# Kernel optimization log

Hardware: AMD Instinct MI355X
Metric: run time of the kernel (lower is better)

The kernel has to match this reference:

```python
import jax, jax.numpy as jnp
import numpy as np

N_NODES = 100000
N_EDGES = 1000000
NEG_SLOPE = 0.2


def gat_conv(x, src, dst, W, al, ar, b, res, activation):
    """DGL-style GATConv. res is None (no residual), 'id' (identity residual), or a [in,H*D] matrix."""
    H, D = al.shape
    n = x.shape[0]
    feat = (x @ W).reshape(n, H, D)                      # [N,H,D]
    el = jnp.einsum('nhd,hd->nh', feat, al)              # [N,H]
    er = jnp.einsum('nhd,hd->nh', feat, ar)              # [N,H]
    e = jax.nn.leaky_relu(el[src] + er[dst], NEG_SLOPE)  # [E,H]
    # edge softmax over incoming edges of each dst node
    m = jax.lax.stop_gradient(jax.ops.segment_max(e, dst, num_segments=n))
    ex = jnp.exp(e - m[dst])
    s = jax.ops.segment_sum(ex, dst, num_segments=n)
    alpha = ex / s[dst]                                  # [E,H]
    out = jax.ops.segment_sum(feat[src] * alpha[:, :, None], dst, num_segments=n)  # [N,H,D]
    if res == 'id':
        out = out + x.reshape(n, H, D)
    elif res is not None:
        out = out + (x @ res).reshape(n, H, D)
    out = out + b.reshape(1, H, D)
    if activation is not None:
        out = activation(out)
    return out


def setup_inputs() -> dict:
    key = jax.random.key(0)
    ks = jax.random.split(key, 20)
    F_IN, HID = 128, 32
    H1, H2, H3 = 4, 4, 1
    C = 40
    sc = 0.1
    inp = {
        'x':   jax.random.normal(ks[0], (N_NODES, F_IN), dtype=jnp.float32),
        'src': jax.random.randint(ks[1], (N_EDGES,), 0, N_NODES, dtype=jnp.int32),
        'dst': jax.random.randint(ks[2], (N_EDGES,), 0, N_NODES, dtype=jnp.int32),
        # layer 1: in=128 -> H1*HID=128, no residual, elu
        'W1':  sc * jax.random.normal(ks[3], (F_IN, H1 * HID), dtype=jnp.float32),
        'al1': sc * jax.random.normal(ks[4], (H1, HID), dtype=jnp.float32),
        'ar1': sc * jax.random.normal(ks[5], (H1, HID), dtype=jnp.float32),
        'b1':  jnp.zeros((H1 * HID,), dtype=jnp.float32),
        # layer 2: in=128 -> H2*HID=128, identity residual, elu
        'W2':  sc * jax.random.normal(ks[6], (H1 * HID, H2 * HID), dtype=jnp.float32),
        'al2': sc * jax.random.normal(ks[7], (H2, HID), dtype=jnp.float32),
        'ar2': sc * jax.random.normal(ks[8], (H2, HID), dtype=jnp.float32),
        'b2':  jnp.zeros((H2 * HID,), dtype=jnp.float32),
        # layer 3 (output): in=128 -> H3*HID=32, projected residual, no activation
        'W3':  sc * jax.random.normal(ks[9], (H2 * HID, H3 * HID), dtype=jnp.float32),
        'al3': sc * jax.random.normal(ks[10], (H3, HID), dtype=jnp.float32),
        'ar3': sc * jax.random.normal(ks[11], (H3, HID), dtype=jnp.float32),
        'b3':  jnp.zeros((H3 * HID,), dtype=jnp.float32),
        'res3': sc * jax.random.normal(ks[12], (H2 * HID, H3 * HID), dtype=jnp.float32),
        # final classifier
        'Wfc': sc * jax.random.normal(ks[13], (HID, C), dtype=jnp.float32),
        'bfc': jnp.zeros((C,), dtype=jnp.float32),
    }
    return inp


def reference(x, src, dst, W1, al1, ar1, b1, W2, al2, ar2, b2, W3, al3, ar3, b3, res3, Wfc, bfc):
    n = x.shape[0]
    h = gat_conv(x, src, dst, W1, al1, ar1, b1, None, jax.nn.elu).reshape(n, -1)   # [N, 128]
    h = gat_conv(h, src, dst, W2, al2, ar2, b2, 'id', jax.nn.elu).reshape(n, -1)   # [N, 128]
    h = gat_conv(h, src, dst, W3, al3, ar3, b3, res3, None).mean(axis=1)           # [N, 32]
    return h @ Wfc + bfc                                                           # [N, 40]
```

## Files before the change

kernel.cpp:

```cpp
#include <hip/hip_runtime.h>
#include <cstdint>
#include <cstddef>

#define NN 100000
#define NE 1000000
#define GEMM_BLOCKS 1563
#define TICKET_BLOCKS 3907
#define CAST_BLOCKS 12500
#define LOG2E 1.4426950408896340736f

typedef unsigned int uint;
typedef unsigned short ushort;
typedef __attribute__((ext_vector_type(8))) short bfrag;
typedef __attribute__((ext_vector_type(4))) float f32x4;

__device__ __forceinline__ ushort f2bf(float f){
  uint u = __float_as_uint(f);
  u += 0x7fffu + ((u >> 16) & 1u);
  return (ushort)(u >> 16);
}
__device__ __forceinline__ float bflo(uint p){ return __uint_as_float(p << 16); }
__device__ __forceinline__ float bfhi(uint p){ return __uint_as_float(p & 0xffff0000u); }


__global__ __launch_bounds__(256) void k_scan_local(const int* __restrict__ cnt, int* __restrict__ rowptr,
                                                    int* __restrict__ bsum){
  __shared__ int sm[256];
  int t = threadIdx.x;
  int i = blockIdx.x*256 + t;
  int v = (i < NN) ? cnt[i] : 0;
  sm[t] = v;
  __syncthreads();
  for (int off=1; off<256; off<<=1){
    int u = (t>=off) ? sm[t-off] : 0;
    __syncthreads();
    sm[t] += u;
    __syncthreads();
  }
  if (i < NN) rowptr[i] = sm[t] - v;
  if (t == 255) bsum[blockIdx.x] = sm[255];
}

__global__ __launch_bounds__(512) void k_scan_bsum(const int* __restrict__ bsum, int* __restrict__ boff, int nb){
  __shared__ int sm[512];
  int t = threadIdx.x;
  int v = (t < nb) ? bsum[t] : 0;
  sm[t] = v;
  __syncthreads();
  for (int off=1; off<512; off<<=1){
    int u = (t>=off) ? sm[t-off] : 0;
    __syncthreads();
    sm[t] += u;
    __syncthreads();
  }
  if (t < nb) boff[t] = sm[t] - v;
}

__global__ __launch_bounds__(256) void k_scan_add(int* __restrict__ rowptr, const int* __restrict__ boff){
  int i = blockIdx.x*256 + threadIdx.x;
  if (i < NN) rowptr[i] += boff[i>>8];
  else if (i == NN) rowptr[NN] = NE;
}


__global__ __launch_bounds__(256) void k_dhist(const int* __restrict__ rowptr, int* __restrict__ dbin){
  __shared__ int lh[256];
  int t = threadIdx.x;
  lh[t] = 0;
  __syncthreads();
  int n = blockIdx.x*256 + t;
  if (n < NN){
    int deg = rowptr[n+1] - rowptr[n];
    atomicAdd(&lh[deg > 255 ? 255 : deg], 1);
  }
  __syncthreads();
  if (lh[t] > 0) atomicAdd(&dbin[t], lh[t]);
}

__global__ __launch_bounds__(256) void k_dscan(int* __restrict__ dbin){
  __shared__ int sm[256];
  int t = threadIdx.x;
  int v = dbin[t];
  sm[t] = v;
  __syncthreads();
  for (int off=1; off<256; off<<=1){
    int u = (t>=off) ? sm[t-off] : 0;
    __syncthreads();
    sm[t] += u;
    __syncthreads();
  }
  dbin[t] = sm[t] - v;
}

__global__ __launch_bounds__(256) void k_dscat(const int* __restrict__ rowptr, int* __restrict__ dbin,
                                               int* __restrict__ perm){
  __shared__ int lh[256];
  __shared__ int lbase[256];
  int t = threadIdx.x;
  lh[t] = 0;
  __syncthreads();
  int n = blockIdx.x*256 + t;
  int bin = -1, lticket = 0;
  if (n < NN){
    int deg = rowptr[n+1] - rowptr[n];
    bin = deg > 255 ? 255 : deg;
    lticket = atomicAdd(&lh[bin], 1);
  }
  __syncthreads();
  if (lh[t] > 0) lbase[t] = atomicAdd(&dbin[t], lh[t]);
  __syncthreads();
  if (n < NN) perm[lbase[bin] + lticket] = n;
}


__device__ __forceinline__ void bfrag_body(const float* __restrict__ B1, const float* __restrict__ B2,
                                           int n1, int n2, int NT, ushort* __restrict__ out, int i){
  if (i >= NT*4*64) return;
  int l = i & 63, ks = (i>>6)&3, nt = i>>8;
  int col = nt*16 + (l&15);
  int k0  = ks*32 + (l>>4)*8;
  const float* B; int stride, c;
  if (col < n1){ B = B1; stride = n1; c = col; }
  else         { B = B2; stride = n2; c = col - n1; }
  ushort v[8];
  #pragma unroll
  for (int j=0;j<8;j++) v[j] = f2bf(B[(size_t)(k0+j)*stride + c]);
  uint4 pk;
  pk.x = (uint)v[0] | ((uint)v[1]<<16);
  pk.y = (uint)v[2] | ((uint)v[3]<<16);
  pk.z = (uint)v[4] | ((uint)v[5]<<16);
  pk.w = (uint)v[6] | ((uint)v[7]<<16);
  *(uint4*)(out + (size_t)i*8) = pk;
}

__global__ __launch_bounds__(256) void k_prep(const float* __restrict__ x, ushort* __restrict__ xb,
                                              const float* __restrict__ W1, const float* __restrict__ W2,
                                              const float* __restrict__ W3, const float* __restrict__ res3,
                                              ushort* __restrict__ Bf1, ushort* __restrict__ Bf2,
                                              ushort* __restrict__ Bf3,
                                              const int* __restrict__ dst, int* __restrict__ cnt,
                                              int* __restrict__ tick){
  int bid = blockIdx.x, t = threadIdx.x;
  if (bid < CAST_BLOCKS){
    int i = bid*256 + t;
    float4 v = ((const float4*)x)[i];
    uint2 p;
    p.x = (uint)f2bf(v.x) | ((uint)f2bf(v.y)<<16);
    p.y = (uint)f2bf(v.z) | ((uint)f2bf(v.w)<<16);
    ((uint2*)xb)[i] = p;
  } else if (bid < CAST_BLOCKS + 20){
    int r = bid - CAST_BLOCKS;
    if (r < 8)       bfrag_body(W1, nullptr, 128, 0, 8, Bf1, r*256 + t);
    else if (r < 16) bfrag_body(W2, nullptr, 128, 0, 8, Bf2, (r-8)*256 + t);
    else             bfrag_body(W3, res3,    32, 32, 4, Bf3, (r-16)*256 + t);
  } else {
    int e = (bid - CAST_BLOCKS - 20)*256 + t;
    if (e < NE) tick[e] = atomicAdd(&cnt[dst[e]], 1);
  }
}


template<int NT, int NTF, int H>
__device__ __forceinline__ void gemm_body(int bid, const ushort* __restrict__ Ab, const ushort* __restrict__ Bf,
                                          ushort* __restrict__ featb, float* __restrict__ Cres,
                                          const float* __restrict__ al, const float* __restrict__ ar,
                                          float* __restrict__ el, float* __restrict__ er, int M){
  __shared__ ushort Bs[NT*2048];
  int t = threadIdx.x;
  #pragma unroll
  for (int i=0; i<NT; ++i)
    ((uint4*)Bs)[i*256 + t] = ((const uint4*)Bf)[i*256 + t];
  __syncthreads();

  int l = t & 63, w = t >> 6;
  int rw = bid*64 + w*16;
  int c = l & 15, g = l >> 4;

  f32x4 acc[NT];
  #pragma unroll
  for (int nt=0;nt<NT;nt++) acc[nt] = (f32x4){0.f,0.f,0.f,0.f};

  int rowA = rw + c; if (rowA >= M) rowA = M-1;
  const ushort* Ap = Ab + (size_t)rowA*128 + g*8;
  const bfrag* Bp = (const bfrag*)Bs;

  #pragma unroll
  for (int ks=0; ks<4; ++ks){
    bfrag a = *(const bfrag*)(Ap + ks*32);
    #pragma unroll
    for (int nt=0; nt<NT; ++nt){
      bfrag b = Bp[(nt*4+ks)*64 + l];
      acc[nt] = __builtin_amdgcn_mfma_f32_16x16x32_bf16(a, b, acc[nt], 0, 0, 0);
    }
  }

  float alv[H][2], arv[H][2];
  #pragma unroll
  for (int h=0;h<H;h++){
    alv[h][0]=al[h*32+c]*LOG2E;    arv[h][0]=ar[h*32+c]*LOG2E;
    alv[h][1]=al[h*32+16+c]*LOG2E; arv[h][1]=ar[h*32+16+c]*LOG2E;
  }

  #pragma unroll
  for (int reg=0; reg<4; ++reg){
    int row = rw + g*4 + reg;
    bool ok = row < M;
    #pragma unroll
    for (int h=0;h<H;h++){
      float pl = acc[2*h][reg]*alv[h][0] + acc[2*h+1][reg]*alv[h][1];
      float pr = acc[2*h][reg]*arv[h][0] + acc[2*h+1][reg]*arv[h][1];
      #pragma unroll
      for (int off=1; off<16; off<<=1){ pl += __shfl_xor(pl,off); pr += __shfl_xor(pr,off); }
      if (ok && c==0){ el[(size_t)row*H + h] = pl; er[(size_t)row*H + h] = pr; }
    }
    if (ok){
      #pragma unroll
      for (int nt=0; nt<NTF; ++nt)
        featb[(size_t)row*(NTF*16) + nt*16 + c] = f2bf(acc[nt][reg]);
      #pragma unroll
      for (int nt=NTF; nt<NT; ++nt)
        Cres[(size_t)row*((NT-NTF)*16) + (nt-NTF)*16 + c] = acc[nt][reg];
    }
  }
}

template<int NT, int NTF, int H>
__global__ __launch_bounds__(256) void k_gemm_mfma(const ushort* __restrict__ Ab, const ushort* __restrict__ Bf,
                                                   ushort* __restrict__ featb, float* __restrict__ Cres,
                                                   const float* __restrict__ al, const float* __restrict__ ar,
                                                   float* __restrict__ el, float* __restrict__ er, int M){
  gemm_body<NT,NTF,H>(blockIdx.x, Ab, Bf, featb, Cres, al, ar, el, er, M);
}

__global__ __launch_bounds__(256) void k_gemm1_place(const ushort* __restrict__ xb, const ushort* __restrict__ Bf1,
                                                     ushort* __restrict__ featb,
                                                     const float* __restrict__ al, const float* __restrict__ ar,
                                                     float* __restrict__ el, float* __restrict__ er,
                                                     const int* __restrict__ src, const int* __restrict__ dst,
                                                     const int* __restrict__ rowptr, const int* __restrict__ tick,
                                                     int* __restrict__ csr){
  int bid = blockIdx.x;
  if (bid < GEMM_BLOCKS){
    gemm_body<8,8,4>(bid, xb, Bf1, featb, nullptr, al, ar, el, er, NN);
  } else {
    int e = (bid - GEMM_BLOCKS)*256 + threadIdx.x;
    if (e < NE){
      int d = dst[e];
      csr[rowptr[d] + tick[e]] = src[e];
    }
  }
}


template<int RK>
__global__ __launch_bounds__(256) void k_agg4(const int* __restrict__ rowptr, const int* __restrict__ csr,
                                              const int* __restrict__ perm,
                                              const ushort* __restrict__ feat,
                                              const float* __restrict__ el, const float* __restrict__ er,
                                              const void* __restrict__ res, const float* __restrict__ bias,
                                              ushort* __restrict__ out, int act){
  int t = threadIdx.x;
  int l15 = t & 15;
  int node = perm[blockIdx.x*16 + (t>>4)];

  int beg = rowptr[node], deg = rowptr[node+1] - beg;
  int hm = l15 >> 2;
  float erh = er[(size_t)node*4 + hm];
  const int* cp = csr + beg;
  uint fo = (uint)l15*8u;

  float ssum = 0.f;
  float a0=0.f,a1=0.f,a2=0.f,a3=0.f,a4=0.f,a5=0.f,a6=0.f,a7=0.f;

  int ei = 0;
  for (; ei+2 <= deg; ei += 2){
    int s0 = cp[ei], s1 = cp[ei+1];
    uint4 p0 = *(const uint4*)(feat + ((uint)s0*128u + fo));
    uint4 p1 = *(const uint4*)(feat + ((uint)s1*128u + fo));
    float v0 = el[(uint)s0*4u + hm] + erh; v0 = fmaxf(v0, 0.2f*v0);
    float v1 = el[(uint)s1*4u + hm] + erh; v1 = fmaxf(v1, 0.2f*v1);
    float w0 = __builtin_amdgcn_exp2f(v0);
    float w1 = __builtin_amdgcn_exp2f(v1);
    ssum += w0 + w1;
    a0 += w0*bflo(p0.x) + w1*bflo(p1.x);
    a1 += w0*bfhi(p0.x) + w1*bfhi(p1.x);
    a2 += w0*bflo(p0.y) + w1*bflo(p1.y);
    a3 += w0*bfhi(p0.y) + w1*bfhi(p1.y);
    a4 += w0*bflo(p0.z) + w1*bflo(p1.z);
    a5 += w0*bfhi(p0.z) + w1*bfhi(p1.z);
    a6 += w0*bflo(p0.w) + w1*bflo(p1.w);
    a7 += w0*bfhi(p0.w) + w1*bfhi(p1.w);
  }
  if (ei < deg){
    int s0 = cp[ei];
    uint4 p0 = *(const uint4*)(feat + ((uint)s0*128u + fo));
    float v0 = el[(uint)s0*4u + hm] + erh; v0 = fmaxf(v0, 0.2f*v0);
    float w0 = __builtin_amdgcn_exp2f(v0);
    ssum += w0;
    a0 += w0*bflo(p0.x); a1 += w0*bfhi(p0.x);
    a2 += w0*bflo(p0.y); a3 += w0*bfhi(p0.y);
    a4 += w0*bflo(p0.z); a5 += w0*bfhi(p0.z);
    a6 += w0*bflo(p0.w); a7 += w0*bfhi(p0.w);
  }

  float inv = (deg > 0) ? 1.f/ssum : 0.f;
  float o0=a0*inv, o1=a1*inv, o2=a2*inv, o3=a3*inv;
  float o4=a4*inv, o5=a5*inv, o6=a6*inv, o7=a7*inv;
  if (RK == 1){
    uint4 rv = *(const uint4*)((const ushort*)res + (size_t)node*128 + fo);
    o0 += bflo(rv.x); o1 += bfhi(rv.x); o2 += bflo(rv.y); o3 += bfhi(rv.y);
    o4 += bflo(rv.z); o5 += bfhi(rv.z); o6 += bflo(rv.w); o7 += bfhi(rv.w);
  }
  float4 bv0 = *(const float4*)(bias + l15*8);
  float4 bv1 = *(const float4*)(bias + l15*8 + 4);
  o0 += bv0.x; o1 += bv0.y; o2 += bv0.z; o3 += bv0.w;
  o4 += bv1.x; o5 += bv1.y; o6 += bv1.z; o7 += bv1.w;
  if (act){
    o0 = (o0>0.f)?o0:__expf(o0)-1.f;
    o1 = (o1>0.f)?o1:__expf(o1)-1.f;
    o2 = (o2>0.f)?o2:__expf(o2)-1.f;
    o3 = (o3>0.f)?o3:__expf(o3)-1.f;
    o4 = (o4>0.f)?o4:__expf(o4)-1.f;
    o5 = (o5>0.f)?o5:__expf(o5)-1.f;
    o6 = (o6>0.f)?o6:__expf(o6)-1.f;
    o7 = (o7>0.f)?o7:__expf(o7)-1.f;
  }
  uint4 pk;
  pk.x = (uint)f2bf(o0) | ((uint)f2bf(o1)<<16);
  pk.y = (uint)f2bf(o2) | ((uint)f2bf(o3)<<16);
  pk.z = (uint)f2bf(o4) | ((uint)f2bf(o5)<<16);
  pk.w = (uint)f2bf(o6) | ((uint)f2bf(o7)<<16);
  *(uint4*)(out + (size_t)node*128 + fo) = pk;
}


__global__ __launch_bounds__(256) void k_agg1(const int* __restrict__ rowptr, const int* __restrict__ csr,
                                              const int* __restrict__ perm,
                                              const ushort* __restrict__ feat,
                                              const float* __restrict__ el, const float* __restrict__ er,
                                              const float* __restrict__ res, const float* __restrict__ bias,
                                              float* __restrict__ h3){
  int t = threadIdx.x;
  int l7 = t & 7;
  int node = perm[blockIdx.x*32 + (t>>3)];

  int beg = rowptr[node], deg = rowptr[node+1] - beg;
  float er0 = er[node];
  const int* cp = csr + beg;
  uint fo = (uint)l7*4u;

  float ssum = 0.f, a0=0.f, a1=0.f, a2=0.f, a3=0.f;
  int ei = 0;
  for (; ei+2 <= deg; ei += 2){
    int s0 = cp[ei], s1 = cp[ei+1];
    uint2 p0 = *(const uint2*)(feat + ((uint)s0*32u + fo));
    uint2 p1 = *(const uint2*)(feat + ((uint)s1*32u + fo));
    float v0 = el[s0] + er0; v0 = fmaxf(v0, 0.2f*v0);
    float v1 = el[s1] + er0; v1 = fmaxf(v1, 0.2f*v1);
    float w0 = __builtin_amdgcn_exp2f(v0);
    float w1 = __builtin_amdgcn_exp2f(v1);
    ssum += w0 + w1;
    a0 += w0*bflo(p0.x) + w1*bflo(p1.x);
    a1 += w0*bfhi(p0.x) + w1*bfhi(p1.x);
    a2 += w0*bflo(p0.y) + w1*bflo(p1.y);
    a3 += w0*bfhi(p0.y) + w1*bfhi(p1.y);
  }
  if (ei < deg){
    int s0 = cp[ei];
    uint2 p0 = *(const uint2*)(feat + ((uint)s0*32u + fo));
    float v0 = el[s0] + er0; v0 = fmaxf(v0, 0.2f*v0);
    float w0 = __builtin_amdgcn_exp2f(v0);
    ssum += w0;
    a0 += w0*bflo(p0.x); a1 += w0*bfhi(p0.x);
    a2 += w0*bflo(p0.y); a3 += w0*bfhi(p0.y);
  }

  float inv = (deg > 0) ? 1.f/ssum : 0.f;
  float4 rv = *(const float4*)(res + (size_t)node*32 + fo);
  float4 bv = *(const float4*)(bias + fo);
  float4 ov;
  ov.x = a0*inv + rv.x + bv.x;
  ov.y = a1*inv + rv.y + bv.y;
  ov.z = a2*inv + rv.z + bv.z;
  ov.w = a3*inv + rv.w + bv.w;
  *(float4*)(h3 + (size_t)node*32 + fo) = ov;
}


__global__ __launch_bounds__(256) void k_fc(const float* __restrict__ h, const float* __restrict__ W,
                                            const float* __restrict__ b, float* __restrict__ out){
  __shared__ float Ws[32*40];
  __shared__ float Hs[64][33];
  __shared__ float bs[40];
  int t = threadIdx.x;
  for (int i=t; i<1280; i+=256) Ws[i] = W[i];
  if (t < 40) bs[t] = b[t];
  int n0 = blockIdx.x*64;
  for (int idx=t; idx<512; idx+=256){
    int r = idx>>3, c4 = idx&7;
    float4 v;
    if (n0 + r < NN) v = *(const float4*)(h + (size_t)(n0+r)*32 + c4*4);
    else v = make_float4(0.f,0.f,0.f,0.f);
    Hs[r][c4*4+0]=v.x; Hs[r][c4*4+1]=v.y; Hs[r][c4*4+2]=v.z; Hs[r][c4*4+3]=v.w;
  }
  __syncthreads();
  int n = t>>2, cg = t&3;
  float acc[10];
  #pragma unroll
  for (int j=0;j<10;j++) acc[j] = 0.f;
  #pragma unroll
  for (int k=0;k<32;k++){
    float hv = Hs[n][k];
    #pragma unroll
    for (int j=0;j<10;j++) acc[j] += hv * Ws[k*40 + cg + 4*j];
  }
  int row = n0 + n;
  if (row < NN){
    #pragma unroll
    for (int j=0;j<10;j++) out[(size_t)row*40 + cg + 4*j] = acc[j] + bs[cg+4*j];
  }
}


extern "C" void kernel_launch(void* const* d_in, const int* in_sizes, int n_in,
                              void* d_out, int out_size, void* d_ws, size_t ws_size,
                              hipStream_t stream){
  const float* x    = (const float*)d_in[0];
  const int*   src  = (const int*)  d_in[1];
  const int*   dst  = (const int*)  d_in[2];
  const float* W1   = (const float*)d_in[3];
  const float* al1  = (const float*)d_in[4];
  const float* ar1  = (const float*)d_in[5];
  const float* b1   = (const float*)d_in[6];
  const float* W2   = (const float*)d_in[7];
  const float* al2  = (const float*)d_in[8];
  const float* ar2  = (const float*)d_in[9];
  const float* b2   = (const float*)d_in[10];
  const float* W3   = (const float*)d_in[11];
  const float* al3  = (const float*)d_in[12];
  const float* ar3  = (const float*)d_in[13];
  const float* b3   = (const float*)d_in[14];
  const float* res3 = (const float*)d_in[15];
  const float* Wfc  = (const float*)d_in[16];
  const float* bfc  = (const float*)d_in[17];
  float* out = (float*)d_out;

  char* ws = (char*)d_ws;
  size_t o = 0;
  auto alloc = [&](size_t bytes)->char*{
    char* p = ws + o;
    o += (bytes + 255) & ~(size_t)255;
    return p;
  };
  int*    rowptr = (int*)   alloc((size_t)(NN+1)*4);
  int*    cnt    = (int*)   alloc((size_t)NN*4);
  int*    bsum   = (int*)   alloc(512*4);
  int*    boff   = (int*)   alloc(512*4);
  int*    dbin   = (int*)   alloc(256*4);
  int*    perm   = (int*)   alloc((size_t)NN*4);
  int*    tick   = (int*)   alloc((size_t)NE*4);
  int*    csr    = (int*)   alloc((size_t)NE*4);
  float*  el     = (float*) alloc((size_t)NN*4*4);
  float*  er     = (float*) alloc((size_t)NN*4*4);
  ushort* xb     = (ushort*)alloc((size_t)NN*128*2);
  ushort* featb  = (ushort*)alloc((size_t)NN*128*2);
  ushort* h1b    = (ushort*)alloc((size_t)NN*128*2);
  ushort* h2b    = (ushort*)alloc((size_t)NN*128*2);
  float*  res3p  = (float*) alloc((size_t)NN*32*4);
  float*  h3     = (float*) alloc((size_t)NN*32*4);
  ushort* Bf1    = (ushort*)alloc((size_t)8*4*64*8*2);
  ushort* Bf2    = (ushort*)alloc((size_t)8*4*64*8*2);
  ushort* Bf3    = (ushort*)alloc((size_t)4*4*64*8*2);
  (void)ws_size; (void)n_in; (void)in_sizes; (void)out_size;

  hipMemsetAsync(cnt, 0, (size_t)NN*4, stream);
  hipMemsetAsync(dbin, 0, 256*4, stream);
  k_prep<<<CAST_BLOCKS+20+TICKET_BLOCKS, 256, 0, stream>>>(x, xb, W1, W2, W3, res3,
                                                           Bf1, Bf2, Bf3, dst, cnt, tick);
  int nb = (NN+255)/256;
  k_scan_local<<<nb, 256, 0, stream>>>(cnt, rowptr, bsum);
  k_scan_bsum<<<1, 512, 0, stream>>>(bsum, boff, nb);
  k_scan_add<<<(NN+1+255)/256, 256, 0, stream>>>(rowptr, boff);

  k_dhist<<<nb, 256, 0, stream>>>(rowptr, dbin);
  k_dscan<<<1, 256, 0, stream>>>(dbin);
  k_dscat<<<nb, 256, 0, stream>>>(rowptr, dbin, perm);

  k_gemm1_place<<<GEMM_BLOCKS+TICKET_BLOCKS, 256, 0, stream>>>(xb, Bf1, featb, al1, ar1, el, er,
                                                               src, dst, rowptr, tick, csr);
  k_agg4<0><<<NN/16, 256, 0, stream>>>(rowptr, csr, perm, featb, el, er, nullptr, b1, h1b, 1);

  k_gemm_mfma<8,8,4><<<GEMM_BLOCKS, 256, 0, stream>>>(h1b, Bf2, featb, nullptr, al2, ar2, el, er, NN);
  k_agg4<1><<<NN/16, 256, 0, stream>>>(rowptr, csr, perm, featb, el, er, h1b, b2, h2b, 1);

  k_gemm_mfma<4,2,1><<<GEMM_BLOCKS, 256, 0, stream>>>(h2b, Bf3, featb, res3p, al3, ar3, el, er, NN);
  k_agg1<<<NN/32, 256, 0, stream>>>(rowptr, csr, perm, featb, el, er, res3p, b3, h3);
  k_fc<<<GEMM_BLOCKS, 256, 0, stream>>>(h3, Wfc, bfc, out);
}
```

Measured before the change: 298.1 us.

## Split degree counters into four sub-slots and unroll aggregation edge loop by four

The per-destination atomic degree counter is split into four sub-counters chosen by edge index modulo four. This spreads atomic contention across separate addresses, and the scan kernel computes sub-offsets so that CSR placement stays correct. Separately, the layer aggregation loop now handles four edges per iteration, giving more outstanding gathers. The cost is extra memory for the counter and offset arrays, an extra offset read during placement, and more registers in the aggregation kernel.

New measurement: 301.8 us. About the same (+1.2%).

```diff
diff --git a/kernel.cpp b/kernel.cpp
--- a/kernel.cpp
+++ b/kernel.cpp
@@ -23,12 +23,19 @@
 __device__ __forceinline__ float bfhi(uint p){ return __uint_as_float(p & 0xffff0000u); }
 
 
-__global__ __launch_bounds__(256) void k_scan_local(const int* __restrict__ cnt, int* __restrict__ rowptr,
-                                                    int* __restrict__ bsum){
+__global__ __launch_bounds__(256) void k_scan_local(const int* __restrict__ cnt4, int* __restrict__ shoff,
+                                                    int* __restrict__ rowptr, int* __restrict__ bsum){
   __shared__ int sm[256];
   int t = threadIdx.x;
   int i = blockIdx.x*256 + t;
-  int v = (i < NN) ? cnt[i] : 0;
+  int v = 0;
+  if (i < NN){
+    int4 c = ((const int4*)cnt4)[i];
+    v = c.x + c.y + c.z + c.w;
+    int4 so;
+    so.x = 0; so.y = c.x; so.z = c.x + c.y; so.w = c.x + c.y + c.z;
+    ((int4*)shoff)[i] = so;
+  }
   sm[t] = v;
   __syncthreads();
   for (int off=1; off<256; off<<=1){
@@ -138,7 +145,7 @@
                                               const float* __restrict__ W3, const float* __restrict__ res3,
                                               ushort* __restrict__ Bf1, ushort* __restrict__ Bf2,
                                               ushort* __restrict__ Bf3,
-                                              const int* __restrict__ dst, int* __restrict__ cnt,
+                                              const int* __restrict__ dst, int* __restrict__ cnt4,
                                               int* __restrict__ tick){
   int bid = blockIdx.x, t = threadIdx.x;
   if (bid < CAST_BLOCKS){
@@ -155,7 +162,7 @@
     else             bfrag_body(W3, res3,    32, 32, 4, Bf3, (r-16)*256 + t);
   } else {
     int e = (bid - CAST_BLOCKS - 20)*256 + t;
-    if (e < NE) tick[e] = atomicAdd(&cnt[dst[e]], 1);
+    if (e < NE) tick[e] = atomicAdd(&cnt4[(uint)dst[e]*4u + (e & 3)], 1);
   }
 }
 
@@ -237,8 +244,8 @@
                                                      const float* __restrict__ al, const float* __restrict__ ar,
                                                      float* __restrict__ el, float* __restrict__ er,
                                                      const int* __restrict__ src, const int* __restrict__ dst,
-                                                     const int* __restrict__ rowptr, const int* __restrict__ tick,
-                                                     int* __restrict__ csr){
+                                                     const int* __restrict__ rowptr, const int* __restrict__ shoff,
+                                                     const int* __restrict__ tick, int* __restrict__ csr){
   int bid = blockIdx.x;
   if (bid < GEMM_BLOCKS){
     gemm_body<8,8,4>(bid, xb, Bf1, featb, nullptr, al, ar, el, er, NN);
@@ -246,7 +253,7 @@
     int e = (bid - GEMM_BLOCKS)*256 + threadIdx.x;
     if (e < NE){
       int d = dst[e];
-      csr[rowptr[d] + tick[e]] = src[e];
+      csr[rowptr[d] + shoff[(uint)d*4u + (e & 3)] + tick[e]] = src[e];
     }
   }
 }
@@ -273,25 +280,31 @@
   float a0=0.f,a1=0.f,a2=0.f,a3=0.f,a4=0.f,a5=0.f,a6=0.f,a7=0.f;
 
   int ei = 0;
-  for (; ei+2 <= deg; ei += 2){
-    int s0 = cp[ei], s1 = cp[ei+1];
+  for (; ei+4 <= deg; ei += 4){
+    int s0 = cp[ei], s1 = cp[ei+1], s2 = cp[ei+2], s3 = cp[ei+3];
     uint4 p0 = *(const uint4*)(feat + ((uint)s0*128u + fo));
     uint4 p1 = *(const uint4*)(feat + ((uint)s1*128u + fo));
+    uint4 p2 = *(const uint4*)(feat + ((uint)s2*128u + fo));
+    uint4 p3 = *(const uint4*)(feat + ((uint)s3*128u + fo));
     float v0 = el[(uint)s0*4u + hm] + erh; v0 = fmaxf(v0, 0.2f*v0);
     float v1 = el[(uint)s1*4u + hm] + erh; v1 = fmaxf(v1, 0.2f*v1);
+    float v2 = el[(uint)s2*4u + hm] + erh; v2 = fmaxf(v2, 0.2f*v2);
+    float v3 = el[(uint)s3*4u + hm] + erh; v3 = fmaxf(v3, 0.2f*v3);
     float w0 = __builtin_amdgcn_exp2f(v0);
     float w1 = __builtin_amdgcn_exp2f(v1);
-    ssum += w0 + w1;
-    a0 += w0*bflo(p0.x) + w1*bflo(p1.x);
-    a1 += w0*bfhi(p0.x) + w1*bfhi(p1.x);
-    a2 += w0*bflo(p0.y) + w1*bflo(p1.y);
-    a3 += w0*bfhi(p0.y) + w1*bfhi(p1.y);
-    a4 += w0*bflo(p0.z) + w1*bflo(p1.z);
-    a5 += w0*bfhi(p0.z) + w1*bfhi(p1.z);
-    a6 += w0*bflo(p0.w) + w1*bflo(p1.w);
-    a7 += w0*bfhi(p0.w) + w1*bfhi(p1.w);
-  }
-  if (ei < deg){
+    float w2 = __builtin_amdgcn_exp2f(v2);
+    float w3 = __builtin_amdgcn_exp2f(v3);
+    ssum += (w0 + w1) + (w2 + w3);
+    a0 += w0*bflo(p0.x) + w1*bflo(p1.x) + w2*bflo(p2.x) + w3*bflo(p3.x);
+    a1 += w0*bfhi(p0.x) + w1*bfhi(p1.x) + w2*bfhi(p2.x) + w3*bfhi(p3.x);
+    a2 += w0*bflo(p0.y) + w1*bflo(p1.y) + w2*bflo(p2.y) + w3*bflo(p3.y);
+    a3 += w0*bfhi(p0.y) + w1*bfhi(p1.y) + w2*bfhi(p2.y) + w3*bfhi(p3.y);
+    a4 += w0*bflo(p0.z) + w1*bflo(p1.z) + w2*bflo(p2.z) + w3*bflo(p3.z);
+    a5 += w0*bfhi(p0.z) + w1*bfhi(p1.z) + w2*bfhi(p2.z) + w3*bfhi(p3.z);
+    a6 += w0*bflo(p0.w) + w1*bflo(p1.w) + w2*bflo(p2.w) + w3*bflo(p3.w);
+    a7 += w0*bfhi(p0.w) + w1*bfhi(p1.w) + w2*bfhi(p2.w) + w3*bfhi(p3.w);
+  }
+  for (; ei < deg; ++ei){
     int s0 = cp[ei];
     uint4 p0 = *(const uint4*)(feat + ((uint)s0*128u + fo));
     float v0 = el[(uint)s0*4u + hm] + erh; v0 = fmaxf(v0, 0.2f*v0);
@@ -453,7 +466,8 @@
     return p;
   };
   int*    rowptr = (int*)   alloc((size_t)(NN+1)*4);
-  int*    cnt    = (int*)   alloc((size_t)NN*4);
+  int*    cnt4   = (int*)   alloc((size_t)NN*4*4);
+  int*    shoff  = (int*)   alloc((size_t)NN*4*4);
   int*    bsum   = (int*)   alloc(512*4);
   int*    boff   = (int*)   alloc(512*4);
   int*    dbin   = (int*)   alloc(256*4);
@@ -473,12 +487,12 @@
   ushort* Bf3    = (ushort*)alloc((size_t)4*4*64*8*2);
   (void)ws_size; (void)n_in; (void)in_sizes; (void)out_size;
 
-  hipMemsetAsync(cnt, 0, (size_t)NN*4, stream);
+  hipMemsetAsync(cnt4, 0, (size_t)NN*4*4, stream);
   hipMemsetAsync(dbin, 0, 256*4, stream);
   k_prep<<<CAST_BLOCKS+20+TICKET_BLOCKS, 256, 0, stream>>>(x, xb, W1, W2, W3, res3,
-                                                           Bf1, Bf2, Bf3, dst, cnt, tick);
+                                                           Bf1, Bf2, Bf3, dst, cnt4, tick);
   int nb = (NN+255)/256;
-  k_scan_local<<<nb, 256, 0, stream>>>(cnt, rowptr, bsum);
+  k_scan_local<<<nb, 256, 0, stream>>>(cnt4, shoff, rowptr, bsum);
   k_scan_bsum<<<1, 512, 0, stream>>>(bsum, boff, nb);
   k_scan_add<<<(NN+1+255)/256, 256, 0, stream>>>(rowptr, boff);
 
@@ -487,7 +501,7 @@
   k_dscat<<<nb, 256, 0, stream>>>(rowptr, dbin, perm);
 
   k_gemm1_place<<<GEMM_BLOCKS+TICKET_BLOCKS, 256, 0, stream>>>(xb, Bf1, featb, al1, ar1, el, er,
-                                                               src, dst, rowptr, tick, csr);
+                                                               src, dst, rowptr, shoff, tick, csr);
   k_agg4<0><<<NN/16, 256, 0, stream>>>(rowptr, csr, perm, featb, el, er, nullptr, b1, h1b, 1);
 
   k_gemm_mfma<8,8,4><<<GEMM_BLOCKS, 256, 0, stream>>>(h1b, Bf2, featb, nullptr, al2, ar2, el, er, NN);
```
